# Optimization experiments

Hardware: AMD Instinct MI355X
Metric: run time of the kernel (lower is better)

Reference implementation:

```python
import jax, jax.numpy as jnp
import numpy as np

D = 1024
NUM_HEADS = 16
HEAD_DIM = D // NUM_HEADS
INIT_VALUES = 1e-4


def setup_inputs() -> dict:
    key = jax.random.key(0)
    ks = jax.random.split(key, 24)
    s = 0.02
    inp = {
        "v": jax.random.normal(ks[0], (8, 2048, D), dtype=jnp.float32),
        "l": jax.random.normal(ks[1], (8, 512, D), dtype=jnp.float32),
        "ln_v_g": jnp.ones((D,), jnp.float32),
        "ln_v_b": jnp.zeros((D,), jnp.float32),
        "ln_l_g": jnp.ones((D,), jnp.float32),
        "ln_l_b": jnp.zeros((D,), jnp.float32),
        "gamma_v": jnp.full((D,), INIT_VALUES, jnp.float32),
        "gamma_l": jnp.full((D,), INIT_VALUES, jnp.float32),
    }
    names = ["Wq_v2l", "Wk_v2l", "Wv_v2l", "Wo_v2l", "Wq_l2v", "Wk_l2v", "Wv_l2v", "Wo_l2v"]
    for i, n in enumerate(names):
        inp[n] = jax.random.normal(ks[2 + i], (D, D), dtype=jnp.float32) * s
        inp[n.replace("W", "b")] = jnp.zeros((D,), jnp.float32)
    return inp


def layer_norm(x, g, b, eps=1e-5):
    mu = jnp.mean(x, axis=-1, keepdims=True)
    var = jnp.var(x, axis=-1, keepdims=True)
    return (x - mu) * jax.lax.rsqrt(var + eps) * g + b


def mha(q_in, k_in, v_in, Wq, bq, Wk, bk, Wv, bv, Wo, bo):
    B, Sq, _ = q_in.shape
    Sk = k_in.shape[1]
    # torch Linear: x @ W.T + b
    q = (q_in @ Wq.T + bq).reshape(B, Sq, NUM_HEADS, HEAD_DIM)
    k = (k_in @ Wk.T + bk).reshape(B, Sk, NUM_HEADS, HEAD_DIM)
    v = (v_in @ Wv.T + bv).reshape(B, Sk, NUM_HEADS, HEAD_DIM)
    scores = jnp.einsum("bqhd,bkhd->bhqk", q, k) / np.sqrt(HEAD_DIM).astype(np.float32)
    attn = jax.nn.softmax(scores, axis=-1)
    ctx = jnp.einsum("bhqk,bkhd->bqhd", attn, v).reshape(B, Sq, D)
    return ctx @ Wo.T + bo


def reference(v, l, ln_v_g, ln_v_b, ln_l_g, ln_l_b, gamma_v, gamma_l,
              Wq_v2l, bq_v2l, Wk_v2l, bk_v2l, Wv_v2l, bv_v2l, Wo_v2l, bo_v2l,
              Wq_l2v, bq_l2v, Wk_l2v, bk_l2v, Wv_l2v, bv_l2v, Wo_l2v, bo_l2v):
    # eval mode: dropout and drop_path are identity
    v_norm = layer_norm(v, ln_v_g, ln_v_b)
    l_norm = layer_norm(l, ln_l_g, ln_l_b)
    updated_v = mha(v_norm, l_norm, l_norm,
                    Wq_v2l, bq_v2l, Wk_v2l, bk_v2l, Wv_v2l, bv_v2l, Wo_v2l, bo_v2l)
    updated_l = mha(l_norm, v_norm, v_norm,
                    Wq_l2v, bq_l2v, Wk_l2v, bk_l2v, Wv_l2v, bv_l2v, Wo_l2v, bo_l2v)
    v_out = v + gamma_v * updated_v
    l_out = l + gamma_l * updated_l
    return (v_out, l_out)
```

## Files before the change

### kernel.cpp

```cpp
#include <hip/hip_runtime.h>
#include <hip/hip_bf16.h>
#include <stdint.h>

typedef __bf16 bf16x8 __attribute__((ext_vector_type(8)));
typedef float f32x4 __attribute__((ext_vector_type(4)));
typedef float f32x16 __attribute__((ext_vector_type(16)));
typedef uint32_t u32x4 __attribute__((ext_vector_type(4)));
typedef unsigned short u16;

typedef __attribute__((address_space(1))) void as1_void;
typedef __attribute__((address_space(3))) void as3_void;

#define BAR() __builtin_amdgcn_s_barrier()
#define VMCNT(n) asm volatile("s_waitcnt vmcnt(" #n ")" ::: "memory")
#define LGKM0() asm volatile("s_waitcnt lgkmcnt(0)" ::: "memory")

__device__ __forceinline__ u16 f2bf(float f) {
  uint32_t u = __float_as_uint(f);
  u += 0x7fffu + ((u >> 16) & 1u);
  return (u16)(u >> 16);
}

__device__ __forceinline__ uint32_t cvtpk(float lo, float hi) {
  uint32_t r;
  asm("v_cvt_pk_bf16_f32 %0, %1, %2" : "=v"(r) : "v"(lo), "v"(hi));
  return r;
}

__global__ __launch_bounds__(256) void cvt8_kernel(
    const float4* s0, const float4* s1, const float4* s2, const float4* s3,
    const float4* s4, const float4* s5, const float4* s6, const float4* s7,
    ushort4* d0, ushort4* d1, ushort4* d2, ushort4* d3,
    ushort4* d4, ushort4* d5, ushort4* d6, ushort4* d7) {
  const float4* s; ushort4* d;
  switch (blockIdx.y) {
    case 0: s = s0; d = d0; break;
    case 1: s = s1; d = d1; break;
    case 2: s = s2; d = d2; break;
    case 3: s = s3; d = d3; break;
    case 4: s = s4; d = d4; break;
    case 5: s = s5; d = d5; break;
    case 6: s = s6; d = d6; break;
    default: s = s7; d = d7; break;
  }
  int i = blockIdx.x * 256 + threadIdx.x;
  float4 v = s[i];
  ushort4 o;
  o.x = f2bf(v.x); o.y = f2bf(v.y); o.z = f2bf(v.z); o.w = f2bf(v.w);
  d[i] = o;
}

__global__ __launch_bounds__(256) void ln_kernel(const float* __restrict__ x,
                                                 const float* __restrict__ g,
                                                 const float* __restrict__ b,
                                                 u16* __restrict__ out) {
  int row = blockIdx.x;
  int t = threadIdx.x;
  const float4* xr = (const float4*)(x + (size_t)row * 1024);
  float4 v = xr[t];
  float s = v.x + v.y + v.z + v.w;
  float s2 = v.x * v.x + v.y * v.y + v.z * v.z + v.w * v.w;
#pragma unroll
  for (int off = 1; off < 64; off <<= 1) {
    s += __shfl_xor(s, off);
    s2 += __shfl_xor(s2, off);
  }
  __shared__ float red[8];
  int wv = t >> 6;
  if ((t & 63) == 0) { red[wv] = s; red[4 + wv] = s2; }
  __syncthreads();
  s = red[0] + red[1] + red[2] + red[3];
  s2 = red[4] + red[5] + red[6] + red[7];
  float mu = s * (1.0f / 1024.0f);
  float var = s2 * (1.0f / 1024.0f) - mu * mu;
  float rstd = rsqrtf(var + 1e-5f);
  const float4 gv = ((const float4*)g)[t];
  const float4 bv = ((const float4*)b)[t];
  ushort4 o;
  o.x = f2bf((v.x - mu) * rstd * gv.x + bv.x);
  o.y = f2bf((v.y - mu) * rstd * gv.y + bv.y);
  o.z = f2bf((v.z - mu) * rstd * gv.z + bv.z);
  o.w = f2bf((v.w - mu) * rstd * gv.w + bv.w);
  ((ushort4*)out)[(size_t)row * 256 + t] = o;
}

template <int MODE>
__global__ __launch_bounds__(256) void gemm_kernel(
    const u16* __restrict__ A, const u16* __restrict__ W,
    const float* __restrict__ bias,
    u16* __restrict__ outb, float* __restrict__ outf,
    const float* __restrict__ res, const float* __restrict__ gamma,
    int sk_shift, float ascale) {
  const int K = 1024, N = 1024;
  int m0 = blockIdx.x * 128, n0 = blockIdx.y * 128;
  int t = threadIdx.x, lane = t & 63, wv = t >> 6;
  int wr = wv >> 1, wc = wv & 1;
  int lr = lane & 15, lk = (lane >> 4) * 8;
  __shared__ u16 As[128 * 32];
  __shared__ u16 Ws[128 * 32];
  f32x4 acc[4][4] = {};
  for (int kt = 0; kt < K / 32; ++kt) {
#pragma unroll
    for (int i = 0; i < 2; ++i) {
      int c = i * 256 + t;
      int row = c >> 2, k8 = (c & 3) << 3;
      const u16* ga = A + (size_t)(m0 + row) * K + kt * 32 + k8;
      const u16* gw = W + (size_t)(n0 + row) * K + kt * 32 + k8;
      __builtin_amdgcn_global_load_lds((const as1_void*)ga, (as3_void*)(As + c * 8), 16, 0, 0);
      __builtin_amdgcn_global_load_lds((const as1_void*)gw, (as3_void*)(Ws + c * 8), 16, 0, 0);
    }
    __syncthreads();
    bf16x8 af[4], wf[4];
#pragma unroll
    for (int m = 0; m < 4; ++m)
      af[m] = *(const bf16x8*)(As + (wr * 64 + m * 16 + lr) * 32 + lk);
#pragma unroll
    for (int n = 0; n < 4; ++n)
      wf[n] = *(const bf16x8*)(Ws + (wc * 64 + n * 16 + lr) * 32 + lk);
#pragma unroll
    for (int m = 0; m < 4; ++m)
#pragma unroll
      for (int n = 0; n < 4; ++n)
        acc[m][n] = __builtin_amdgcn_mfma_f32_16x16x32_bf16(af[m], wf[n], acc[m][n], 0, 0, 0);
    __syncthreads();
  }
  int rowb = m0 + wr * 64 + (lane >> 4) * 4;
#pragma unroll
  for (int m = 0; m < 4; ++m) {
#pragma unroll
    for (int n = 0; n < 4; ++n) {
      int col = n0 + wc * 64 + n * 16 + lr;
      float bcol = bias[col];
#pragma unroll
      for (int r = 0; r < 4; ++r) {
        int row = rowb + m * 16 + r;
        float val = (acc[m][n][r] + bcol) * ascale;
        if (MODE == 0) {
          outb[(size_t)row * N + col] = f2bf(val);
        } else if (MODE == 1) {
          size_t idx = (size_t)row * N + col;
          outf[idx] = res[idx] + gamma[col] * val;
        } else {
          int bb = row >> sk_shift;
          int ss = row & ((1 << sk_shift) - 1);
          int h = col >> 6, d = col & 63;
          outb[((((size_t)bb * 16 + h) * 64 + d) << sk_shift) + ss] = f2bf(val);
        }
      }
    }
  }
}

template <int MODE>
__global__ __launch_bounds__(512, 2) void gemm256_kernel(
    const u16* __restrict__ A, const u16* __restrict__ W,
    const float* __restrict__ bias,
    u16* __restrict__ outb, float* __restrict__ outf,
    const float* __restrict__ res, const float* __restrict__ gamma,
    int mtiles, int sk_shift, float ascale) {
  const int K = 1024, N = 1024;
  int nwg = mtiles * 4;
  int cpx = nwg >> 3;
  int bid = blockIdx.x;
  int swz = (bid & 7) * cpx + (bid >> 3);
  int mt = swz >> 2, nt = swz & 3;
  int m0 = mt * 256, n0 = nt * 256;

  int t = threadIdx.x, lane = t & 63, wv = t >> 6;
  int wm = wv >> 2, wn = wv & 3;
  int lr = lane & 15, lg = lane >> 4;
  int sa0 = ((lg) ^ (lr & 7)) * 8;
  int sa1 = ((4 + lg) ^ (lr & 7)) * 8;

  __shared__ u16 AB[2][2][256 * 64];
  u16* ldsA0 = &AB[0][0][0];
  u16* ldsB0 = &AB[0][1][0];
  u16* ldsA1 = &AB[1][0][0];
  u16* ldsB1 = &AB[1][1][0];

  int r0 = t >> 3, c0 = t & 7;
  int cs0 = c0 ^ (r0 & 7);
  const u16* gA0 = A + (size_t)(m0 + r0) * K + cs0 * 8;
  const u16* gA1 = gA0 + (size_t)64 * K;
  const u16* gB0 = W + (size_t)(n0 + r0) * K + cs0 * 8;
  const u16* gB1 = gB0 + (size_t)64 * K;

  auto STG = [&](u16* ldsbase, const u16* g0, const u16* g1, int half, int kt) {
    __builtin_amdgcn_global_load_lds(
        (const as1_void*)(g0 + (size_t)half * 128 * K + kt * 64),
        (as3_void*)(ldsbase + (half * 128 + r0) * 64 + c0 * 8), 16, 0, 0);
    __builtin_amdgcn_global_load_lds(
        (const as1_void*)(g1 + (size_t)half * 128 * K + kt * 64),
        (as3_void*)(ldsbase + (half * 128 + r0 + 64) * 64 + c0 * 8), 16, 0, 0);
  };

  f32x4 acc[8][4] = {};
  bf16x8 aX[4][2], bX[2][2], bY[2][2];

  auto LD_A = [&](const u16* base, int mo) {
#pragma unroll
    for (int m = 0; m < 4; ++m) {
      const u16* rp = base + (wm * 128 + (mo + m) * 16 + lr) * 64;
      aX[m][0] = *(const bf16x8*)(rp + sa0);
      aX[m][1] = *(const bf16x8*)(rp + sa1);
    }
  };
  auto LD_B = [&](bf16x8 (&dst)[2][2], const u16* base, int no) {
#pragma unroll
    for (int n = 0; n < 2; ++n) {
      const u16* rp = base + (wn * 64 + (no + n) * 16 + lr) * 64;
      dst[n][0] = *(const bf16x8*)(rp + sa0);
      dst[n][1] = *(const bf16x8*)(rp + sa1);
    }
  };
  auto QD = [&](bf16x8 (&bf)[2][2], int mo, int no) {
#pragma unroll
    for (int m = 0; m < 4; ++m)
#pragma unroll
      for (int n = 0; n < 2; ++n) {
        acc[mo + m][no + n] = __builtin_amdgcn_mfma_f32_16x16x32_bf16(
            aX[m][0], bf[n][0], acc[mo + m][no + n], 0, 0, 0);
        acc[mo + m][no + n] = __builtin_amdgcn_mfma_f32_16x16x32_bf16(
            aX[m][1], bf[n][1], acc[mo + m][no + n], 0, 0, 0);
      }
  };

  STG(ldsA0, gA0, gA1, 0, 0); STG(ldsA0, gA0, gA1, 1, 0);
  STG(ldsB0, gB0, gB1, 0, 0); STG(ldsB0, gB0, gB1, 1, 0);
  STG(ldsA1, gA0, gA1, 0, 1); STG(ldsA1, gA0, gA1, 1, 1);
  STG(ldsB1, gB0, gB1, 0, 1); STG(ldsB1, gB0, gB1, 1, 1);
  VMCNT(8);
  BAR();

  const int NIT = K / 128;
#pragma unroll 1
  for (int it = 0; it < NIT; ++it) {
    bool st = (it + 1 < NIT);
    int ktA = 2 * it;
    LD_A(ldsA0, 0); LD_B(bX, ldsB0, 0);
    BAR(); LGKM0();
    __builtin_amdgcn_s_setprio(1); QD(bX, 0, 0); __builtin_amdgcn_s_setprio(0);
    BAR();
    LD_B(bY, ldsB0, 2);
    BAR(); LGKM0();
    __builtin_amdgcn_s_setprio(1); QD(bY, 0, 2); __builtin_amdgcn_s_setprio(0);
    BAR();
    LD_A(ldsA0, 4);
    if (st) { STG(ldsB0, gB0, gB1, 0, ktA + 2); STG(ldsB0, gB0, gB1, 1, ktA + 2); }
    BAR(); LGKM0();
    __builtin_amdgcn_s_setprio(1); QD(bY, 4, 2); __builtin_amdgcn_s_setprio(0);
    BAR();
    if (st) { STG(ldsA0, gA0, gA1, 0, ktA + 2); STG(ldsA0, gA0, gA1, 1, ktA + 2); }
    if (st) { VMCNT(8); } else { VMCNT(0); }
    BAR();
    __builtin_amdgcn_s_setprio(1); QD(bX, 4, 0); __builtin_amdgcn_s_setprio(0);
    BAR();
    LD_A(ldsA1, 0); LD_B(bX, ldsB1, 0);
    BAR(); LGKM0();
    __builtin_amdgcn_s_setprio(1); QD(bX, 0, 0); __builtin_amdgcn_s_setprio(0);
    BAR();
    LD_B(bY, ldsB1, 2);
    BAR(); LGKM0();
    __builtin_amdgcn_s_setprio(1); QD(bY, 0, 2); __builtin_amdgcn_s_setprio(0);
    BAR();
    LD_A(ldsA1, 4);
    if (st) { STG(ldsB1, gB0, gB1, 0, ktA + 3); STG(ldsB1, gB0, gB1, 1, ktA + 3); }
    BAR(); LGKM0();
    __builtin_amdgcn_s_setprio(1); QD(bY, 4, 2); __builtin_amdgcn_s_setprio(0);
    BAR();
    if (st) { STG(ldsA1, gA0, gA1, 0, ktA + 3); STG(ldsA1, gA0, gA1, 1, ktA + 3); }
    if (st) { VMCNT(8); }
    BAR();
    __builtin_amdgcn_s_setprio(1); QD(bX, 4, 0); __builtin_amdgcn_s_setprio(0);
    BAR();
  }

  int rowb = m0 + wm * 128 + lg * 4;
#pragma unroll
  for (int mi = 0; mi < 8; ++mi) {
#pragma unroll
    for (int n = 0; n < 4; ++n) {
      int col = n0 + wn * 64 + n * 16 + lr;
      float bcol = bias[col];
#pragma unroll
      for (int r = 0; r < 4; ++r) {
        int row = rowb + mi * 16 + r;
        float val = (acc[mi][n][r] + bcol) * ascale;
        if (MODE == 0) {
          outb[(size_t)row * N + col] = f2bf(val);
        } else if (MODE == 1) {
          size_t idx = (size_t)row * N + col;
          outf[idx] = res[idx] + gamma[col] * val;
        } else {
          int bb = row >> sk_shift;
          int ss = row & ((1 << sk_shift) - 1);
          int h = col >> 6, d = col & 63;
          outb[((((size_t)bb * 16 + h) * 64 + d) << sk_shift) + ss] = f2bf(val);
        }
      }
    }
  }
}

__global__ __launch_bounds__(256, 4) void attn_kernel(
    const u16* __restrict__ Q, const u16* __restrict__ Kmat,
    const u16* __restrict__ Vt, u16* __restrict__ ctx,
    int Sq, int Sk, int nq_shift) {
  int f = blockIdx.x;
  int xcd = f & 7, slot = f >> 3;
  int group = xcd * 16 + (slot >> nq_shift);
  int qt = slot & ((1 << nq_shift) - 1);
  int b = group >> 4, h = group & 15;
  int t = threadIdx.x, lane = t & 63, wv = t >> 6;
  int l31 = lane & 31, hi = lane >> 5;

  __shared__ u16 Ks[2][64 * 64];
  __shared__ u16 Vs[2][64 * 64];

  int q0 = qt * 128 + wv * 32;
  const u16* Qb = Q + (size_t)(b * Sq + q0 + l31) * 1024 + h * 64 + hi * 8;
  bf16x8 qf[4];
#pragma unroll
  for (int ds = 0; ds < 4; ++ds) qf[ds] = *(const bf16x8*)(Qb + ds * 16);

  int trow = t >> 3, tc = t & 7;
  int sc = (tc ^ (trow & 7)) * 8;
  const u16* gk = Kmat + (size_t)(b * Sk + trow) * 1024 + h * 64 + sc;
  const u16* gv = Vt + (size_t)((b * 16 + h) * 64 + trow) * Sk + sc;

  auto STAGE = [&](int buf, int kt) {
    const u16* k0 = gk + (size_t)(kt * 64) * 1024;
    const u16* v0 = gv + kt * 64;
    __builtin_amdgcn_global_load_lds((const as1_void*)k0, (as3_void*)(Ks[buf] + t * 8), 16, 0, 0);
    __builtin_amdgcn_global_load_lds((const as1_void*)(k0 + (size_t)32 * 1024), (as3_void*)(Ks[buf] + 2048 + t * 8), 16, 0, 0);
    __builtin_amdgcn_global_load_lds((const as1_void*)v0, (as3_void*)(Vs[buf] + t * 8), 16, 0, 0);
    __builtin_amdgcn_global_load_lds((const as1_void*)(v0 + (size_t)32 * Sk), (as3_void*)(Vs[buf] + 2048 + t * 8), 16, 0, 0);
  };

  STAGE(0, 0);
  __syncthreads();

  f32x16 acc0 = {}, acc1 = {};
  float m_run = -1e30f, l_run = 0.f;
  int sw = l31 & 7;

  int nt = Sk >> 6;
  for (int kt = 0; kt < nt; ++kt) {
    int cur = kt & 1;
    if (kt + 1 < nt) STAGE(cur ^ 1, kt + 1);
    const u16* kb = Ks[cur];
    f32x16 s0v = {}, s1v = {};
    __builtin_amdgcn_s_setprio(1);
#pragma unroll
    for (int ds = 0; ds < 4; ++ds) {
      int blk = 2 * ds + hi;
      bf16x8 ka0 = *(const bf16x8*)(kb + l31 * 64 + ((blk ^ sw) * 8));
      bf16x8 ka1 = *(const bf16x8*)(kb + (32 + l31) * 64 + ((blk ^ sw) * 8));
      s0v = __builtin_amdgcn_mfma_f32_32x32x16_bf16(ka0, qf[ds], s0v, 0, 0, 0);
      s1v = __builtin_amdgcn_mfma_f32_32x32x16_bf16(ka1, qf[ds], s1v, 0, 0, 0);
    }
    __builtin_amdgcn_s_setprio(0);
    float mx = s0v[0];
#pragma unroll
    for (int i = 1; i < 16; ++i) mx = fmaxf(mx, s0v[i]);
#pragma unroll
    for (int i = 0; i < 16; ++i) mx = fmaxf(mx, s1v[i]);
    mx = fmaxf(mx, __shfl_xor(mx, 32));
    if (__any(mx > m_run + 8.f)) {
      float mnew = fmaxf(m_run, mx);
      float fac = __builtin_amdgcn_exp2f(m_run - mnew);
#pragma unroll
      for (int r = 0; r < 16; ++r) {
        int src = (r & 3) + 8 * (r >> 2) + 4 * hi;
        float fr = __shfl(fac, src);
        acc0[r] *= fr;
        acc1[r] *= fr;
      }
      l_run *= fac;
      m_run = mnew;
    }
    float sum = 0.f;
#pragma unroll
    for (int i = 0; i < 16; ++i) {
      s0v[i] = __builtin_amdgcn_exp2f(s0v[i] - m_run);
      sum += s0v[i];
    }
#pragma unroll
    for (int i = 0; i < 16; ++i) {
      s1v[i] = __builtin_amdgcn_exp2f(s1v[i] - m_run);
      sum += s1v[i];
    }
    sum += __shfl_xor(sum, 32);
    l_run += sum;
    bf16x8 pa[4];
#pragma unroll
    for (int g = 0; g < 2; ++g) {
      const f32x16& s = g ? s1v : s0v;
#pragma unroll
      for (int half = 0; half < 2; ++half) {
        int o = half * 8;
        uint32_t a0 = cvtpk(s[o + 0], s[o + 1]);
        uint32_t a1 = cvtpk(s[o + 2], s[o + 3]);
        uint32_t b0 = cvtpk(s[o + 4], s[o + 5]);
        uint32_t b1 = cvtpk(s[o + 6], s[o + 7]);
        asm("v_permlane32_swap_b32 %0, %1" : "+v"(a0), "+v"(b0));
        asm("v_permlane32_swap_b32 %0, %1" : "+v"(a1), "+v"(b1));
        u32x4 w;
        w[0] = a0; w[1] = a1; w[2] = b0; w[3] = b1;
        pa[g * 2 + half] = __builtin_bit_cast(bf16x8, w);
      }
    }
    const u16* vb = Vs[cur];
    __builtin_amdgcn_s_setprio(1);
#pragma unroll
    for (int ks = 0; ks < 4; ++ks) {
      int blk = 2 * ks + hi;
      bf16x8 vf0 = *(const bf16x8*)(vb + l31 * 64 + ((blk ^ sw) * 8));
      bf16x8 vf1 = *(const bf16x8*)(vb + (32 + l31) * 64 + ((blk ^ sw) * 8));
      acc0 = __builtin_amdgcn_mfma_f32_32x32x16_bf16(pa[ks], vf0, acc0, 0, 0, 0);
      acc1 = __builtin_amdgcn_mfma_f32_32x32x16_bf16(pa[ks], vf1, acc1, 0, 0, 0);
    }
    __builtin_amdgcn_s_setprio(0);
    __syncthreads();
  }
  float linv = 1.0f / l_run;
  u16* cb = ctx + (size_t)(b * Sq + q0) * 1024 + h * 64;
#pragma unroll
  for (int r = 0; r < 16; ++r) {
    int src = (r & 3) + 8 * (r >> 2) + 4 * hi;
    float li = __shfl(linv, src);
    cb[(size_t)src * 1024 + l31] = f2bf(acc0[r] * li);
    cb[(size_t)src * 1024 + 32 + l31] = f2bf(acc1[r] * li);
  }
}

extern "C" void kernel_launch(void* const* d_in, const int* in_sizes, int n_in,
                              void* d_out, int out_size, void* d_ws, size_t ws_size,
                              hipStream_t stream) {
  const float* v = (const float*)d_in[0];
  const float* l = (const float*)d_in[1];
  const float* ln_v_g = (const float*)d_in[2];
  const float* ln_v_b = (const float*)d_in[3];
  const float* ln_l_g = (const float*)d_in[4];
  const float* ln_l_b = (const float*)d_in[5];
  const float* gamma_v = (const float*)d_in[6];
  const float* gamma_l = (const float*)d_in[7];
  const float* Wf[8];
  const float* Bf[8];
  for (int i = 0; i < 8; ++i) {
    Wf[i] = (const float*)d_in[8 + 2 * i];
    Bf[i] = (const float*)d_in[9 + 2 * i];
  }
  float* v_out = (float*)d_out;
  float* l_out = v_out + (size_t)16384 * 1024;

  char* p = (char*)d_ws;
  auto alloc = [&](size_t bytes) {
    char* r = p;
    p += (bytes + 255) & ~(size_t)255;
    return r;
  };
  u16* Wbf[8];
  for (int i = 0; i < 8; ++i) Wbf[i] = (u16*)alloc((size_t)1024 * 1024 * 2);
  u16* vn   = (u16*)alloc((size_t)16384 * 1024 * 2);
  u16* lnm  = (u16*)alloc((size_t)4096 * 1024 * 2);
  u16* bufA = (u16*)alloc((size_t)16384 * 1024 * 2);
  u16* bufB = (u16*)alloc((size_t)4096 * 1024 * 2);
  u16* bufC = (u16*)alloc((size_t)4096 * 1024 * 2);
  u16* bufD = (u16*)alloc((size_t)16384 * 1024 * 2);

  const float QSC = 0.125f * 1.4426950408889634f;

  cvt8_kernel<<<dim3(1024, 8), 256, 0, stream>>>(
      (const float4*)Wf[0], (const float4*)Wf[1], (const float4*)Wf[2], (const float4*)Wf[3],
      (const float4*)Wf[4], (const float4*)Wf[5], (const float4*)Wf[6], (const float4*)Wf[7],
      (ushort4*)Wbf[0], (ushort4*)Wbf[1], (ushort4*)Wbf[2], (ushort4*)Wbf[3],
      (ushort4*)Wbf[4], (ushort4*)Wbf[5], (ushort4*)Wbf[6], (ushort4*)Wbf[7]);
  ln_kernel<<<16384, 256, 0, stream>>>(v, ln_v_g, ln_v_b, vn);
  ln_kernel<<<4096, 256, 0, stream>>>(l, ln_l_g, ln_l_b, lnm);

  dim3 blk(256);
  dim3 blk512(512);
  gemm256_kernel<0><<<dim3(256), blk512, 0, stream>>>(vn, Wbf[0], Bf[0], bufA, nullptr, nullptr, nullptr, 64, 0, QSC);
  gemm_kernel<0><<<dim3(32, 8), blk, 0, stream>>>(lnm, Wbf[1], Bf[1], bufB, nullptr, nullptr, nullptr, 0, 1.0f);
  gemm_kernel<2><<<dim3(32, 8), blk, 0, stream>>>(lnm, Wbf[2], Bf[2], bufC, nullptr, nullptr, nullptr, 9, 1.0f);
  attn_kernel<<<dim3(2048), blk, 0, stream>>>(bufA, bufB, bufC, bufD, 2048, 512, 4);
  gemm256_kernel<1><<<dim3(256), blk512, 0, stream>>>(bufD, Wbf[3], Bf[3], nullptr, v_out, v, gamma_v, 64, 0, 1.0f);
  gemm_kernel<0><<<dim3(32, 8), blk, 0, stream>>>(lnm, Wbf[4], Bf[4], bufB, nullptr, nullptr, nullptr, 0, QSC);
  gemm256_kernel<0><<<dim3(256), blk512, 0, stream>>>(vn, Wbf[5], Bf[5], bufA, nullptr, nullptr, nullptr, 64, 0, 1.0f);
  gemm256_kernel<2><<<dim3(256), blk512, 0, stream>>>(vn, Wbf[6], Bf[6], bufD, nullptr, nullptr, nullptr, 64, 11, 1.0f);
  attn_kernel<<<dim3(512), blk, 0, stream>>>(bufB, bufA, bufD, bufC, 512, 2048, 2);
  gemm_kernel<1><<<dim3(32, 8), blk, 0, stream>>>(bufC, Wbf[7], Bf[7], nullptr, l_out, l, gamma_l, 0, 1.0f);
}
```

Before: 435.0 us.

## Use FP8 GEMMs for large v-side projections and batch small projections into launches

The large 16384-row projections (v-side Q, K and V, plus the v output projection) switch from bf16 to FP8 inputs and weights with fp8 MFMA. The normalized v activations and the attention context written for the v output GEMM are stored as FP8. The small l-side Q, K and V GEMMs are merged into one launch, and the v-side K and V GEMMs share one launch, using a segment descriptor. This halves the operand bytes and raises MFMA throughput for the dominant GEMMs and cuts launch count, at the cost of FP8 quantization error with no per-tensor scaling.

```diff
diff --git a/kernel.cpp b/kernel.cpp
--- a/kernel.cpp
+++ b/kernel.cpp
@@ -7,6 +7,7 @@
 typedef float f32x16 __attribute__((ext_vector_type(16)));
 typedef uint32_t u32x4 __attribute__((ext_vector_type(4)));
 typedef unsigned short u16;
+typedef unsigned char u8;
 
 typedef __attribute__((address_space(1))) void as1_void;
 typedef __attribute__((address_space(3))) void as3_void;
@@ -21,39 +22,54 @@
   return (u16)(u >> 16);
 }
 
-__device__ __forceinline__ uint32_t cvtpk(float lo, float hi) {
-  uint32_t r;
-  asm("v_cvt_pk_bf16_f32 %0, %1, %2" : "=v"(r) : "v"(lo), "v"(hi));
-  return r;
-}
+__device__ __forceinline__ uint32_t pk_fp8x4(float a, float b, float c, float d) {
+  int v = __builtin_amdgcn_cvt_pk_fp8_f32(a, b, 0, false);
+  v = __builtin_amdgcn_cvt_pk_fp8_f32(c, d, v, true);
+  return (uint32_t)v;
+}
+__device__ __forceinline__ u8 f2fp8(float a) {
+  return (u8)(__builtin_amdgcn_cvt_pk_fp8_f32(a, a, 0, false) & 0xff);
+}
+
+struct Seg {
+  const void* W;
+  const float* bias;
+  u16* outb;
+  float* outf;
+  const float* res;
+  const float* gamma;
+  int mode;
+  int sk;
+  float ascale;
+};
 
 __global__ __launch_bounds__(256) void cvt8_kernel(
     const float4* s0, const float4* s1, const float4* s2, const float4* s3,
     const float4* s4, const float4* s5, const float4* s6, const float4* s7,
-    ushort4* d0, ushort4* d1, ushort4* d2, ushort4* d3,
-    ushort4* d4, ushort4* d5, ushort4* d6, ushort4* d7) {
-  const float4* s; ushort4* d;
-  switch (blockIdx.y) {
-    case 0: s = s0; d = d0; break;
-    case 1: s = s1; d = d1; break;
-    case 2: s = s2; d = d2; break;
-    case 3: s = s3; d = d3; break;
-    case 4: s = s4; d = d4; break;
-    case 5: s = s5; d = d5; break;
-    case 6: s = s6; d = d6; break;
-    default: s = s7; d = d7; break;
-  }
+    uint32_t* f0, uint32_t* f1, uint32_t* f2, uint32_t* f3,
+    ushort4* h4, ushort4* h5, ushort4* h6, ushort4* h7) {
   int i = blockIdx.x * 256 + threadIdx.x;
-  float4 v = s[i];
-  ushort4 o;
-  o.x = f2bf(v.x); o.y = f2bf(v.y); o.z = f2bf(v.z); o.w = f2bf(v.w);
-  d[i] = o;
-}
-
+  int y = blockIdx.y;
+  if (y < 4) {
+    const float4* s = (y == 0) ? s0 : (y == 1) ? s1 : (y == 2) ? s2 : s3;
+    uint32_t* d = (y == 0) ? f0 : (y == 1) ? f1 : (y == 2) ? f2 : f3;
+    float4 v = s[i];
+    d[i] = pk_fp8x4(v.x, v.y, v.z, v.w);
+  } else {
+    const float4* s = (y == 4) ? s4 : (y == 5) ? s5 : (y == 6) ? s6 : s7;
+    ushort4* d = (y == 4) ? h4 : (y == 5) ? h5 : (y == 6) ? h6 : h7;
+    float4 v = s[i];
+    ushort4 o;
+    o.x = f2bf(v.x); o.y = f2bf(v.y); o.z = f2bf(v.z); o.w = f2bf(v.w);
+    d[i] = o;
+  }
+}
+
+template <int FP8>
 __global__ __launch_bounds__(256) void ln_kernel(const float* __restrict__ x,
                                                  const float* __restrict__ g,
                                                  const float* __restrict__ b,
-                                                 u16* __restrict__ out) {
+                                                 void* __restrict__ out) {
   int row = blockIdx.x;
   int t = threadIdx.x;
   const float4* xr = (const float4*)(x + (size_t)row * 1024);
@@ -76,28 +92,33 @@
   float rstd = rsqrtf(var + 1e-5f);
   const float4 gv = ((const float4*)g)[t];
   const float4 bv = ((const float4*)b)[t];
-  ushort4 o;
-  o.x = f2bf((v.x - mu) * rstd * gv.x + bv.x);
-  o.y = f2bf((v.y - mu) * rstd * gv.y + bv.y);
-  o.z = f2bf((v.z - mu) * rstd * gv.z + bv.z);
-  o.w = f2bf((v.w - mu) * rstd * gv.w + bv.w);
-  ((ushort4*)out)[(size_t)row * 256 + t] = o;
-}
-
-template <int MODE>
-__global__ __launch_bounds__(256) void gemm_kernel(
-    const u16* __restrict__ A, const u16* __restrict__ W,
-    const float* __restrict__ bias,
-    u16* __restrict__ outb, float* __restrict__ outf,
-    const float* __restrict__ res, const float* __restrict__ gamma,
-    int sk_shift, float ascale) {
-  const int K = 1024, N = 1024;
-  int m0 = blockIdx.x * 128, n0 = blockIdx.y * 128;
+  float o0 = (v.x - mu) * rstd * gv.x + bv.x;
+  float o1 = (v.y - mu) * rstd * gv.y + bv.y;
+  float o2 = (v.z - mu) * rstd * gv.z + bv.z;
+  float o3 = (v.w - mu) * rstd * gv.w + bv.w;
+  if (FP8) {
+    ((uint32_t*)out)[(size_t)row * 256 + t] = pk_fp8x4(o0, o1, o2, o3);
+  } else {
+    ushort4 o;
+    o.x = f2bf(o0); o.y = f2bf(o1); o.z = f2bf(o2); o.w = f2bf(o3);
+    ((ushort4*)out)[(size_t)row * 256 + t] = o;
+  }
+}
+
+__global__ __launch_bounds__(256) void gemm128_kernel(
+    const u16* __restrict__ A, Seg s0, Seg s1, Seg s2) {
+  const int K = 1024;
+  int m0 = blockIdx.x * 128;
+  int yy = blockIdx.y;
+  int si = yy >> 3;
+  Seg seg = (si == 0) ? s0 : (si == 1) ? s1 : s2;
+  int nl0 = (yy & 7) * 128;
   int t = threadIdx.x, lane = t & 63, wv = t >> 6;
   int wr = wv >> 1, wc = wv & 1;
   int lr = lane & 15, lk = (lane >> 4) * 8;
   __shared__ u16 As[128 * 32];
   __shared__ u16 Ws[128 * 32];
+  const u16* Wb = (const u16*)seg.W;
   f32x4 acc[4][4] = {};
   for (int kt = 0; kt < K / 32; ++kt) {
 #pragma unroll
@@ -105,7 +126,7 @@
       int c = i * 256 + t;
       int row = c >> 2, k8 = (c & 3) << 3;
       const u16* ga = A + (size_t)(m0 + row) * K + kt * 32 + k8;
-      const u16* gw = W + (size_t)(n0 + row) * K + kt * 32 + k8;
+      const u16* gw = Wb + (size_t)(nl0 + row) * K + kt * 32 + k8;
       __builtin_amdgcn_global_load_lds((const as1_void*)ga, (as3_void*)(As + c * 8), 16, 0, 0);
       __builtin_amdgcn_global_load_lds((const as1_void*)gw, (as3_void*)(Ws + c * 8), 16, 0, 0);
     }
@@ -129,107 +150,110 @@
   for (int m = 0; m < 4; ++m) {
 #pragma unroll
     for (int n = 0; n < 4; ++n) {
-      int col = n0 + wc * 64 + n * 16 + lr;
-      float bcol = bias[col];
+      int scol = nl0 + wc * 64 + n * 16 + lr;
+      float bcol = seg.bias[scol];
 #pragma unroll
       for (int r = 0; r < 4; ++r) {
         int row = rowb + m * 16 + r;
-        float val = (acc[m][n][r] + bcol) * ascale;
-        if (MODE == 0) {
-          outb[(size_t)row * N + col] = f2bf(val);
-        } else if (MODE == 1) {
-          size_t idx = (size_t)row * N + col;
-          outf[idx] = res[idx] + gamma[col] * val;
+        float val = (acc[m][n][r] + bcol) * seg.ascale;
+        if (seg.mode == 0) {
+          seg.outb[(size_t)row * 1024 + scol] = f2bf(val);
+        } else if (seg.mode == 1) {
+          size_t idx = (size_t)row * 1024 + scol;
+          seg.outf[idx] = seg.res[idx] + seg.gamma[scol] * val;
         } else {
-          int bb = row >> sk_shift;
-          int ss = row & ((1 << sk_shift) - 1);
-          int h = col >> 6, d = col & 63;
-          outb[((((size_t)bb * 16 + h) * 64 + d) << sk_shift) + ss] = f2bf(val);
+          int bb = row >> seg.sk;
+          int ss = row & ((1 << seg.sk) - 1);
+          int h = scol >> 6, d = scol & 63;
+          seg.outb[((((size_t)bb * 16 + h) * 64 + d) << seg.sk) + ss] = f2bf(val);
         }
       }
     }
   }
 }
 
-template <int MODE>
-__global__ __launch_bounds__(512, 2) void gemm256_kernel(
-    const u16* __restrict__ A, const u16* __restrict__ W,
-    const float* __restrict__ bias,
-    u16* __restrict__ outb, float* __restrict__ outf,
-    const float* __restrict__ res, const float* __restrict__ gamma,
-    int mtiles, int sk_shift, float ascale) {
-  const int K = 1024, N = 1024;
-  int nwg = mtiles * 4;
+__global__ __launch_bounds__(512, 2) void gemm256f8_kernel(
+    const u8* __restrict__ A, Seg s0, Seg s1, Seg s2,
+    int mtiles, int nt_shift) {
+  const int K = 1024;
+  int ntiles = 1 << nt_shift;
+  int nwg = mtiles * ntiles;
   int cpx = nwg >> 3;
   int bid = blockIdx.x;
   int swz = (bid & 7) * cpx + (bid >> 3);
-  int mt = swz >> 2, nt = swz & 3;
-  int m0 = mt * 256, n0 = nt * 256;
+  int mt = swz >> nt_shift, nt = swz & (ntiles - 1);
+  int m0 = mt * 256;
+  int si = nt >> 2;
+  Seg seg = (si == 0) ? s0 : (si == 1) ? s1 : s2;
+  int nl0 = (nt & 3) * 256;
 
   int t = threadIdx.x, lane = t & 63, wv = t >> 6;
   int wm = wv >> 2, wn = wv & 3;
   int lr = lane & 15, lg = lane >> 4;
-  int sa0 = ((lg) ^ (lr & 7)) * 8;
-  int sa1 = ((4 + lg) ^ (lr & 7)) * 8;
-
-  __shared__ u16 AB[2][2][256 * 64];
-  u16* ldsA0 = &AB[0][0][0];
-  u16* ldsB0 = &AB[0][1][0];
-  u16* ldsA1 = &AB[1][0][0];
-  u16* ldsB1 = &AB[1][1][0];
-
-  int r0 = t >> 3, c0 = t & 7;
-  int cs0 = c0 ^ (r0 & 7);
-  const u16* gA0 = A + (size_t)(m0 + r0) * K + cs0 * 8;
-  const u16* gA1 = gA0 + (size_t)64 * K;
-  const u16* gB0 = W + (size_t)(n0 + r0) * K + cs0 * 8;
-  const u16* gB1 = gB0 + (size_t)64 * K;
-
-  auto STG = [&](u16* ldsbase, const u16* g0, const u16* g1, int half, int kt) {
-    __builtin_amdgcn_global_load_lds(
-        (const as1_void*)(g0 + (size_t)half * 128 * K + kt * 64),
-        (as3_void*)(ldsbase + (half * 128 + r0) * 64 + c0 * 8), 16, 0, 0);
-    __builtin_amdgcn_global_load_lds(
-        (const as1_void*)(g1 + (size_t)half * 128 * K + kt * 64),
-        (as3_void*)(ldsbase + (half * 128 + r0 + 64) * 64 + c0 * 8), 16, 0, 0);
+
+  __shared__ u8 AB[2][2][256 * 64];
+  u8* ldsA0 = &AB[0][0][0];
+  u8* ldsB0 = &AB[0][1][0];
+  u8* ldsA1 = &AB[1][0][0];
+  u8* ldsB1 = &AB[1][1][0];
+
+  int r0 = t >> 2, c0 = t & 3;
+  int cs0 = (c0 ^ (r0 & 3)) * 16;
+  const u8* gA = A + (size_t)(m0 + r0) * K + cs0;
+  const u8* gB = (const u8*)seg.W + (size_t)(nl0 + r0) * K + cs0;
+
+  auto STG_A = [&](u8* base, int kt) {
+    __builtin_amdgcn_global_load_lds((const as1_void*)(gA + kt * 64),
+                                     (as3_void*)(base + t * 16), 16, 0, 0);
+    __builtin_amdgcn_global_load_lds((const as1_void*)(gA + (size_t)128 * K + kt * 64),
+                                     (as3_void*)(base + 8192 + t * 16), 16, 0, 0);
+  };
+  auto STG_B = [&](u8* base, int kt) {
+    __builtin_amdgcn_global_load_lds((const as1_void*)(gB + kt * 64),
+                                     (as3_void*)(base + t * 16), 16, 0, 0);
+    __builtin_amdgcn_global_load_lds((const as1_void*)(gB + (size_t)128 * K + kt * 64),
+                                     (as3_void*)(base + 8192 + t * 16), 16, 0, 0);
   };
 
   f32x4 acc[8][4] = {};
-  bf16x8 aX[4][2], bX[2][2], bY[2][2];
-
-  auto LD_A = [&](const u16* base, int mo) {
+  long aX[4][2], bX[2][2], bY[2][2];
+  int gq0 = lg >> 1, gsub = (lg & 1) * 8;
+
+  auto LD_A = [&](const u8* base, int mo) {
 #pragma unroll
     for (int m = 0; m < 4; ++m) {
-      const u16* rp = base + (wm * 128 + (mo + m) * 16 + lr) * 64;
-      aX[m][0] = *(const bf16x8*)(rp + sa0);
-      aX[m][1] = *(const bf16x8*)(rp + sa1);
-    }
-  };
-  auto LD_B = [&](bf16x8 (&dst)[2][2], const u16* base, int no) {
+      int row = wm * 128 + (mo + m) * 16 + lr;
+      const u8* rp = base + row * 64;
+      int sw = row & 3;
+      aX[m][0] = *(const long*)(rp + ((gq0 ^ sw) * 16) + gsub);
+      aX[m][1] = *(const long*)(rp + (((2 + gq0) ^ sw) * 16) + gsub);
+    }
+  };
+  auto LD_B = [&](long (&dst)[2][2], const u8* base, int no) {
 #pragma unroll
     for (int n = 0; n < 2; ++n) {
-      const u16* rp = base + (wn * 64 + (no + n) * 16 + lr) * 64;
-      dst[n][0] = *(const bf16x8*)(rp + sa0);
-      dst[n][1] = *(const bf16x8*)(rp + sa1);
-    }
-  };
-  auto QD = [&](bf16x8 (&bf)[2][2], int mo, int no) {
+      int row = wn * 64 + (no + n) * 16 + lr;
+      const u8* rp = base + row * 64;
+      int sw = row & 3;
+      dst[n][0] = *(const long*)(rp + ((gq0 ^ sw) * 16) + gsub);
+      dst[n][1] = *(const long*)(rp + (((2 + gq0) ^ sw) * 16) + gsub);
+    }
+  };
+  auto QD = [&](long (&bf)[2][2], int mo, int no) {
 #pragma unroll
     for (int m = 0; m < 4; ++m)
 #pragma unroll
       for (int n = 0; n < 2; ++n) {
-        acc[mo + m][no + n] = __builtin_amdgcn_mfma_f32_16x16x32_bf16(
+        acc[mo + m][no + n] = __builtin_amdgcn_mfma_f32_16x16x32_fp8_fp8(
             aX[m][0], bf[n][0], acc[mo + m][no + n], 0, 0, 0);
-        acc[mo + m][no + n] = __builtin_amdgcn_mfma_f32_16x16x32_bf16(
+        acc[mo + m][no + n] = __builtin_amdgcn_mfma_f32_16x16x32_fp8_fp8(
             aX[m][1], bf[n][1], acc[mo + m][no + n], 0, 0, 0);
       }
   };
 
-  STG(ldsA0, gA0, gA1, 0, 0); STG(ldsA0, gA0, gA1, 1, 0);
-  STG(ldsB0, gB0, gB1, 0, 0); STG(ldsB0, gB0, gB1, 1, 0);
-  STG(ldsA1, gA0, gA1, 0, 1); STG(ldsA1, gA0, gA1, 1, 1);
-  STG(ldsB1, gB0, gB1, 0, 1); STG(ldsB1, gB0, gB1, 1, 1);
-  VMCNT(8);
+  STG_A(ldsA0, 0); STG_B(ldsB0, 0);
+  STG_A(ldsA1, 1); STG_B(ldsB1, 1);
+  VMCNT(4);
   BAR();
 
   const int NIT = K / 128;
@@ -246,12 +270,11 @@
     __builtin_amdgcn_s_setprio(1); QD(bY, 0, 2); __builtin_amdgcn_s_setprio(0);
     BAR();
     LD_A(ldsA0, 4);
-    if (st) { STG(ldsB0, gB0, gB1, 0, ktA + 2); STG(ldsB0, gB0, gB1, 1, ktA + 2); }
+    if (st) STG_B(ldsB0, ktA + 2);
     BAR(); LGKM0();
     __builtin_amdgcn_s_setprio(1); QD(bY, 4, 2); __builtin_amdgcn_s_setprio(0);
     BAR();
-    if (st) { STG(ldsA0, gA0, gA1, 0, ktA + 2); STG(ldsA0, gA0, gA1, 1, ktA + 2); }
-    if (st) { VMCNT(8); } else { VMCNT(0); }
+    if (st) { STG_A(ldsA0, ktA + 2); VMCNT(4); } else { VMCNT(0); }
     BAR();
     __builtin_amdgcn_s_setprio(1); QD(bX, 4, 0); __builtin_amdgcn_s_setprio(0);
     BAR();
@@ -264,12 +287,11 @@
     __builtin_amdgcn_s_setprio(1); QD(bY, 0, 2); __builtin_amdgcn_s_setprio(0);
     BAR();
     LD_A(ldsA1, 4);
-    if (st) { STG(ldsB1, gB0, gB1, 0, ktA + 3); STG(ldsB1, gB0, gB1, 1, ktA + 3); }
+    if (st) STG_B(ldsB1, ktA + 3);
     BAR(); LGKM0();
     __builtin_amdgcn_s_setprio(1); QD(bY, 4, 2); __builtin_amdgcn_s_setprio(0);
     BAR();
-    if (st) { STG(ldsA1, gA0, gA1, 0, ktA + 3); STG(ldsA1, gA0, gA1, 1, ktA + 3); }
-    if (st) { VMCNT(8); }
+    if (st) { STG_A(ldsA1, ktA + 3); VMCNT(4); }
     BAR();
     __builtin_amdgcn_s_setprio(1); QD(bX, 4, 0); __builtin_amdgcn_s_setprio(0);
     BAR();
@@ -280,22 +302,22 @@
   for (int mi = 0; mi < 8; ++mi) {
 #pragma unroll
     for (int n = 0; n < 4; ++n) {
-      int col = n0 + wn * 64 + n * 16 + lr;
-      float bcol = bias[col];
+      int scol = nl0 + wn * 64 + n * 16 + lr;
+      float bcol = seg.bias[scol];
 #pragma unroll
       for (int r = 0; r < 4; ++r) {
         int row = rowb + mi * 16 + r;
-        float val = (acc[mi][n][r] + bcol) * ascale;
-        if (MODE == 0) {
-          outb[(size_t)row * N + col] = f2bf(val);
-        } else if (MODE == 1) {
-          size_t idx = (size_t)row * N + col;
-          outf[idx] = res[idx] + gamma[col] * val;
+        float val = (acc[mi][n][r] + bcol) * seg.ascale;
+        if (seg.mode == 0) {
+          seg.outb[(size_t)row * 1024 + scol] = f2bf(val);
+        } else if (seg.mode == 1) {
+          size_t idx = (size_t)row * 1024 + scol;
+          seg.outf[idx] = seg.res[idx] + seg.gamma[scol] * val;
         } else {
-          int bb = row >> sk_shift;
-          int ss = row & ((1 << sk_shift) - 1);
-          int h = col >> 6, d = col & 63;
-          outb[((((size_t)bb * 16 + h) * 64 + d) << sk_shift) + ss] = f2bf(val);
+          int bb = row >> seg.sk;
+          int ss = row & ((1 << seg.sk) - 1);
+          int h = scol >> 6, d = scol & 63;
+          seg.outb[((((size_t)bb * 16 + h) * 64 + d) << seg.sk) + ss] = f2bf(val);
         }
       }
     }
@@ -304,8 +326,8 @@
 
 __global__ __launch_bounds__(256, 4) void attn_kernel(
     const u16* __restrict__ Q, const u16* __restrict__ Kmat,
-    const u16* __restrict__ Vt, u16* __restrict__ ctx,
-    int Sq, int Sk, int nq_shift) {
+    const u16* __restrict__ Vt, void* __restrict__ ctx,
+    int Sq, int Sk, int nq_shift, int fp8out) {
   int f = blockIdx.x;
   int xcd = f & 7, slot = f >> 3;
   int group = xcd * 16 + (slot >> nq_shift);
@@ -399,10 +421,11 @@
 #pragma unroll
       for (int half = 0; half < 2; ++half) {
         int o = half * 8;
-        uint32_t a0 = cvtpk(s[o + 0], s[o + 1]);
-        uint32_t a1 = cvtpk(s[o + 2], s[o + 3]);
-        uint32_t b0 = cvtpk(s[o + 4], s[o + 5]);
-        uint32_t b1 = cvtpk(s[o + 6], s[o + 7]);
+        uint32_t a0, a1, b0, b1;
+        asm("v_cvt_pk_bf16_f32 %0, %1, %2" : "=v"(a0) : "v"(s[o + 0]), "v"(s[o + 1]));
+        asm("v_cvt_pk_bf16_f32 %0, %1, %2" : "=v"(a1) : "v"(s[o + 2]), "v"(s[o + 3]));
+        asm("v_cvt_pk_bf16_f32 %0, %1, %2" : "=v"(b0) : "v"(s[o + 4]), "v"(s[o + 5]));
+        asm("v_cvt_pk_bf16_f32 %0, %1, %2" : "=v"(b1) : "v"(s[o + 6]), "v"(s[o + 7]));
         asm("v_permlane32_swap_b32 %0, %1" : "+v"(a0), "+v"(b0));
         asm("v_permlane32_swap_b32 %0, %1" : "+v"(a1), "+v"(b1));
         u32x4 w;
@@ -424,13 +447,24 @@
     __syncthreads();
   }
   float linv = 1.0f / l_run;
-  u16* cb = ctx + (size_t)(b * Sq + q0) * 1024 + h * 64;
-#pragma unroll
-  for (int r = 0; r < 16; ++r) {
-    int src = (r & 3) + 8 * (r >> 2) + 4 * hi;
-    float li = __shfl(linv, src);
-    cb[(size_t)src * 1024 + l31] = f2bf(acc0[r] * li);
-    cb[(size_t)src * 1024 + 32 + l31] = f2bf(acc1[r] * li);
+  if (fp8out) {
+    u8* cb = (u8*)ctx + (size_t)(b * Sq + q0) * 1024 + h * 64;
+#pragma unroll
+    for (int r = 0; r < 16; ++r) {
+      int src = (r & 3) + 8 * (r >> 2) + 4 * hi;
+      float li = __shfl(linv, src);
+      cb[(size_t)src * 1024 + l31] = f2fp8(acc0[r] * li);
+      cb[(size_t)src * 1024 + 32 + l31] = f2fp8(acc1[r] * li);
+    }
+  } else {
+    u16* cb = (u16*)ctx + (size_t)(b * Sq + q0) * 1024 + h * 64;
+#pragma unroll
+    for (int r = 0; r < 16; ++r) {
+      int src = (r & 3) + 8 * (r >> 2) + 4 * hi;
+      float li = __shfl(linv, src);
+      cb[(size_t)src * 1024 + l31] = f2bf(acc0[r] * li);
+      cb[(size_t)src * 1024 + 32 + l31] = f2bf(acc1[r] * li);
+    }
   }
 }
 
@@ -460,35 +494,57 @@
     p += (bytes + 255) & ~(size_t)255;
     return r;
   };
-  u16* Wbf[8];
-  for (int i = 0; i < 8; ++i) Wbf[i] = (u16*)alloc((size_t)1024 * 1024 * 2);
-  u16* vn   = (u16*)alloc((size_t)16384 * 1024 * 2);
+  u8* Wq_v8 = (u8*)alloc(1 << 20);
+  u8* Wk_l8 = (u8*)alloc(1 << 20);
+  u8* Wv_l8 = (u8*)alloc(1 << 20);
+  u8* Wo_v8 = (u8*)alloc(1 << 20);
+  u16* Wk_vb = (u16*)alloc(2 << 20);
+  u16* Wv_vb = (u16*)alloc(2 << 20);
+  u16* Wq_lb = (u16*)alloc(2 << 20);
+  u16* Wo_lb = (u16*)alloc(2 << 20);
+  u8*  vn8  = (u8*)alloc((size_t)16384 * 1024);
   u16* lnm  = (u16*)alloc((size_t)4096 * 1024 * 2);
   u16* bufA = (u16*)alloc((size_t)16384 * 1024 * 2);
   u16* bufB = (u16*)alloc((size_t)4096 * 1024 * 2);
   u16* bufC = (u16*)alloc((size_t)4096 * 1024 * 2);
   u16* bufD = (u16*)alloc((size_t)16384 * 1024 * 2);
+  u16* bufF = (u16*)alloc((size_t)4096 * 1024 * 2);
+  u8*  ctxv = (u8*)alloc((size_t)16384 * 1024);
 
   const float QSC = 0.125f * 1.4426950408889634f;
+  Seg zs = {};
 
   cvt8_kernel<<<dim3(1024, 8), 256, 0, stream>>>(
-      (const float4*)Wf[0], (const float4*)Wf[1], (const float4*)Wf[2], (const float4*)Wf[3],
-      (const float4*)Wf[4], (const float4*)Wf[5], (const float4*)Wf[6], (const float4*)Wf[7],
-      (ushort4*)Wbf[0], (ushort4*)Wbf[1], (ushort4*)Wbf[2], (ushort4*)Wbf[3],
-      (ushort4*)Wbf[4], (ushort4*)Wbf[5], (ushort4*)Wbf[6], (ushort4*)Wbf[7]);
-  ln_kernel<<<16384, 256, 0, stream>>>(v, ln_v_g, ln_v_b, vn);
-  ln_kernel<<<4096, 256, 0, stream>>>(l, ln_l_g, ln_l_b, lnm);
-
-  dim3 blk(256);
-  dim3 blk512(512);
-  gemm256_kernel<0><<<dim3(256), blk512, 0, stream>>>(vn, Wbf[0], Bf[0], bufA, nullptr, nullptr, nullptr, 64, 0, QSC);
-  gemm_kernel<0><<<dim3(32, 8), blk, 0, stream>>>(lnm, Wbf[1], Bf[1], bufB, nullptr, nullptr, nullptr, 0, 1.0f);
-  gemm_kernel<2><<<dim3(32, 8), blk, 0, stream>>>(lnm, Wbf[2], Bf[2], bufC, nullptr, nullptr, nullptr, 9, 1.0f);
-  attn_kernel<<<dim3(2048), blk, 0, stream>>>(bufA, bufB, bufC, bufD, 2048, 512, 4);
-  gemm256_kernel<1><<<dim3(256), blk512, 0, stream>>>(bufD, Wbf[3], Bf[3], nullptr, v_out, v, gamma_v, 64, 0, 1.0f);
-  gemm_kernel<0><<<dim3(32, 8), blk, 0, stream>>>(lnm, Wbf[4], Bf[4], bufB, nullptr, nullptr, nullptr, 0, QSC);
-  gemm256_kernel<0><<<dim3(256), blk512, 0, stream>>>(vn, Wbf[5], Bf[5], bufA, nullptr, nullptr, nullptr, 64, 0, 1.0f);
-  gemm256_kernel<2><<<dim3(256), blk512, 0, stream>>>(vn, Wbf[6], Bf[6], bufD, nullptr, nullptr, nullptr, 64, 11, 1.0f);
-  attn_kernel<<<dim3(512), blk, 0, stream>>>(bufB, bufA, bufD, bufC, 512, 2048, 2);
-  gemm_kernel<1><<<dim3(32, 8), blk, 0, stream>>>(bufC, Wbf[7], Bf[7], nullptr, l_out, l, gamma_l, 0, 1.0f);
-}
+      (const float4*)Wf[0], (const float4*)Wf[5], (const float4*)Wf[6], (const float4*)Wf[3],
+      (const float4*)Wf[1], (const float4*)Wf[2], (const float4*)Wf[4], (const float4*)Wf[7],
+      (uint32_t*)Wq_v8, (uint32_t*)Wk_l8, (uint32_t*)Wv_l8, (uint32_t*)Wo_v8,
+      (ushort4*)Wk_vb, (ushort4*)Wv_vb, (ushort4*)Wq_lb, (ushort4*)Wo_lb);
+  ln_kernel<1><<<16384, 256, 0, stream>>>(v, ln_v_g, ln_v_b, vn8);
+  ln_kernel<0><<<4096, 256, 0, stream>>>(l, ln_l_g, ln_l_b, lnm);
+
+  {
+    Seg a = {Wq_lb, Bf[4], bufB, nullptr, nullptr, nullptr, 0, 0, QSC};
+    Seg b = {Wk_vb, Bf[1], bufF, nullptr, nullptr, nullptr, 0, 0, 1.0f};
+    Seg c = {Wv_vb, Bf[2], bufC, nullptr, nullptr, nullptr, 2, 9, 1.0f};
+    gemm128_kernel<<<dim3(32, 24), 256, 0, stream>>>(lnm, a, b, c);
+  }
+  {
+    Seg q = {Wq_v8, Bf[0], bufA, nullptr, nullptr, nullptr, 0, 0, QSC};
+    gemm256f8_kernel<<<dim3(256), 512, 0, stream>>>(vn8, q, zs, zs, 64, 2);
+  }
+  attn_kernel<<<dim3(2048), 256, 0, stream>>>(bufA, bufF, bufC, ctxv, 2048, 512, 4, 1);
+  {
+    Seg k = {Wk_l8, Bf[5], bufA, nullptr, nullptr, nullptr, 0, 0, 1.0f};
+    Seg vv = {Wv_l8, Bf[6], bufD, nullptr, nullptr, nullptr, 2, 11, 1.0f};
+    gemm256f8_kernel<<<dim3(512), 512, 0, stream>>>(vn8, k, vv, zs, 64, 3);
+  }
+  {
+    Seg o = {Wo_v8, Bf[3], nullptr, v_out, v, gamma_v, 1, 0, 1.0f};
+    gemm256f8_kernel<<<dim3(256), 512, 0, stream>>>(ctxv, o, zs, zs, 64, 2);
+  }
+  attn_kernel<<<dim3(512), 256, 0, stream>>>(bufB, bufA, bufD, lnm, 512, 2048, 2, 0);
+  {
+    Seg o = {Wo_lb, Bf[7], nullptr, l_out, l, gamma_l, 1, 0, 1.0f};
+    gemm128_kernel<<<dim3(32, 8), 256, 0, stream>>>(lnm, o, zs, zs);
+  }
+}
```

Measured after the change: 510.4 us. +17.3%, slower.
